# Kernel optimization log

Hardware: AMD Instinct MI355X
Metric: run time of the kernel (lower is better)

The kernel has to match this reference:

```python
import jax, jax.numpy as jnp
import numpy as np

B, T, D, P = 4, 2048, 1024, 128

def setup_inputs() -> dict:
    key = jax.random.key(0)
    ks = jax.random.split(key, 10)
    inp = {
        "x": jax.random.normal(ks[0], (B, T, D), dtype=jnp.float32),
        "Q_filt": jax.random.normal(ks[1], (P, P), dtype=jnp.float32),
        "K_filt": jax.random.normal(ks[2], (P, P), dtype=jnp.float32),
        "W_in": jax.random.normal(ks[3], (D, P), dtype=jnp.float32) / np.sqrt(D),
        "b_in": jax.random.normal(ks[4], (P,), dtype=jnp.float32) * 0.01,
        "W_v": jax.random.normal(ks[5], (D, P), dtype=jnp.float32) / np.sqrt(D),
        "b_v": jax.random.normal(ks[6], (P,), dtype=jnp.float32) * 0.01,
        "W_o": jax.random.normal(ks[7], (P, D), dtype=jnp.float32) / np.sqrt(P),
        "b_o": jax.random.normal(ks[8], (D,), dtype=jnp.float32) * 0.01,
        "decay": jnp.ones((T,), dtype=jnp.float32),
    }
    return inp

def reference(x, Q_filt, K_filt, W_in, b_in, W_v, b_v, W_o, b_o, decay):
    # x: (B,T,D)
    x_proj = x @ W_in + b_in          # (B,T,P)
    Q = x_proj @ Q_filt               # (B,T,P)
    K = x_proj @ K_filt               # (B,T,P)
    V = x @ W_v + b_v                 # (B,T,P)
    # outer-product state per timestep, scaled by per-step decay
    Z = jnp.einsum('bti,btj->btij', V, K) * decay[None, :, None, None]
    H = jnp.cumsum(Z, axis=1)         # (B,T,P,P) cumulative linear-attn state
    Y = jnp.einsum('bti,btij->btj', Q, H)  # (B,T,P)
    return Y @ W_o + b_o              # (B,T,D)
```

## Files before the change

kernel.cpp:

```cpp
#include <hip/hip_runtime.h>

#define BB 4
#define TT 2048
#define DD 1024
#define PP 128
#define NC 16
#define CH 128

typedef __attribute__((ext_vector_type(8))) short bf16x8;
typedef __attribute__((ext_vector_type(4))) float f32x4;

__device__ inline ushort f2bf(float f) {
  unsigned u = __builtin_bit_cast(unsigned, f);
  u = (u + 0x7FFF + ((u >> 16) & 1)) >> 16;
  return (ushort)u;
}

__device__ inline void gll16(const void* g, void* l) {
  __builtin_amdgcn_global_load_lds(
      (const __attribute__((address_space(1))) void*)g,
      (__attribute__((address_space(3))) void*)l, 16, 0, 0);
}

__device__ inline int swzoff(int row, int kbyte) {
  return row * 256 + (kbyte ^ ((row & 7) << 4));
}
__device__ inline int swz128(int row, int kbyte) {
  return row * 128 + (kbyte ^ ((row & 7) << 4));
}

template <int NI, int NT>
__device__ inline void stage_swz(const ushort* __restrict__ g, int ld, int koff,
                                 char* lds, int tid) {
#pragma unroll
  for (int j = 0; j < NI; ++j) {
    int L = j * (NT * 16) + tid * 16;
    int row = L >> 8;
    int off = (L & 255) ^ ((row & 7) << 4);
    gll16(g + (size_t)row * ld + koff + (off >> 1),
          lds + j * (NT * 16) + ((tid & (NT - 64)) << 4));
  }
}
template <int NI, int NT>
__device__ inline void stage_swz128(const ushort* __restrict__ g, int ld,
                                    int koff, char* lds, int tid) {
#pragma unroll
  for (int j = 0; j < NI; ++j) {
    int L = j * (NT * 16) + tid * 16;
    int row = L >> 7;
    int off = (L & 127) ^ ((row & 7) << 4);
    gll16(g + (size_t)row * ld + koff + (off >> 1),
          lds + j * (NT * 16) + ((tid & (NT - 64)) << 4));
  }
}

__device__ inline bf16x8 ld_swz(const char* lds, int row, int kbyte) {
  return *(const bf16x8*)(lds + swzoff(row, kbyte));
}
__device__ inline bf16x8 ld_swz128(const char* lds, int row, int kbyte) {
  return *(const bf16x8*)(lds + swz128(row, kbyte));
}

__device__ inline bf16x8 pack8(const float4& a, const float4& b) {
  bf16x8 v;
  v[0] = (short)f2bf(a.x); v[1] = (short)f2bf(a.y);
  v[2] = (short)f2bf(a.z); v[3] = (short)f2bf(a.w);
  v[4] = (short)f2bf(b.x); v[5] = (short)f2bf(b.y);
  v[6] = (short)f2bf(b.z); v[7] = (short)f2bf(b.w);
  return v;
}

__global__ __launch_bounds__(256) void prep_t(
    const float* __restrict__ Qf, const float* __restrict__ Kf,
    const float* __restrict__ W_in, const float* __restrict__ b_in,
    const float* __restrict__ W_v, const float* __restrict__ b_v,
    const float* __restrict__ W_o, ushort* __restrict__ WcatT,
    ushort* __restrict__ QKcT, ushort* __restrict__ WoT,
    float* __restrict__ bcat) {
  const int bid = blockIdx.x;
  const int t = threadIdx.x;
  if (bid == 104) {
    bcat[t] = (t < 128) ? b_in[t] : b_v[t - 128];
    return;
  }
  const float* src;
  ushort* dst;
  int ld_src, ld_dst, nn0;
  if (bid < 64) {
    int tn = bid >> 4, tk = bid & 15;
    src = (tn < 2) ? W_in : W_v;
    nn0 = (tn & 1) * 64;
    ld_src = 128;
    src += (size_t)(tk * 64) * 128;
    dst = WcatT + (size_t)(tn * 64) * 1024 + tk * 64;
    ld_dst = 1024;
  } else if (bid < 96) {
    int j = bid - 64, tn = j >> 1, tk = j & 1;
    src = W_o;
    nn0 = tn * 64;
    ld_src = 1024;
    src += (size_t)(tk * 64) * 1024;
    dst = WoT + (size_t)(tn * 64) * 128 + tk * 64;
    ld_dst = 128;
  } else {
    int j = bid - 96, tn = j >> 1, tk = j & 1;
    src = (tn < 2) ? Qf : Kf;
    nn0 = (tn & 1) * 64;
    ld_src = 128;
    src += (size_t)(tk * 64) * 128;
    dst = QKcT + (size_t)(tn * 64) * 128 + tk * 64;
    ld_dst = 128;
  }
  __shared__ ushort Tt[64][68];
  const int kr = t >> 4, nc = (t & 15) * 4;
#pragma unroll
  for (int p = 0; p < 4; ++p) {
    float4 v = *(const float4*)&src[(size_t)(p * 16 + kr) * ld_src + nn0 + nc];
    Tt[p * 16 + kr][nc + 0] = f2bf(v.x);
    Tt[p * 16 + kr][nc + 1] = f2bf(v.y);
    Tt[p * 16 + kr][nc + 2] = f2bf(v.z);
    Tt[p * 16 + kr][nc + 3] = f2bf(v.w);
  }
  __syncthreads();
  const int nr = t >> 4, kc = (t & 15) * 4;
#pragma unroll
  for (int p = 0; p < 4; ++p) {
    ushort4 o;
    o.x = Tt[kc + 0][p * 16 + nr];
    o.y = Tt[kc + 1][p * 16 + nr];
    o.z = Tt[kc + 2][p * 16 + nr];
    o.w = Tt[kc + 3][p * 16 + nr];
    *(ushort4*)&dst[(size_t)(p * 16 + nr) * ld_dst + kc] = o;
  }
}

__global__ __launch_bounds__(512) void gemm_xw(
    const float* __restrict__ x, const ushort* __restrict__ WcatT,
    const ushort* __restrict__ QKcT, const float* __restrict__ bcat,
    const float* __restrict__ decay, ushort* __restrict__ Qb,
    ushort* __restrict__ KdT, ushort* __restrict__ V,
    ushort* __restrict__ VT) {
  __shared__ char sm[81920];
  const int bid = blockIdx.x;
  const int swz = (bid & 7) * 32 + (bid >> 3);
  const int bm = (swz >> 1) * 64;
  const int bn = (swz & 1) * 128;
  const int tid = threadIdx.x, w = tid >> 6, l = tid & 63;
  const int wr = w >> 2, wc = w & 3, lr = l & 15, lk = l >> 4;

  const int arow = tid >> 3;
  const int acol = (tid & 7) * 8;
  const float* Ax = x + (size_t)(bm + arow) * DD + acol;
  const ushort* Bg = WcatT + (size_t)bn * DD;

  float4 ra[2];
  f32x4 z = {0.f, 0.f, 0.f, 0.f};
  f32x4 acc[2][2];
#pragma unroll
  for (int m = 0; m < 2; ++m)
#pragma unroll
    for (int n = 0; n < 2; ++n) acc[m][n] = z;

#define LOADA(t)                                                 \
  {                                                              \
    const float4* p = (const float4*)(Ax + (((t) & 15) << 6));   \
    ra[0] = p[0];                                                \
    ra[1] = p[1];                                                \
  }
#define WRITEA(lds) \
  { *(bf16x8*)((lds) + swz128(arow, acol * 2)) = pack8(ra[0], ra[1]); }

  LOADA(0);
  stage_swz128<2, 512>(Bg, DD, 0, sm + 8192, tid);
  asm volatile("s_waitcnt vmcnt(2)" ::: "memory");
  WRITEA(sm);
  LOADA(1);

  int cur = 0;
  for (int t = 0; t < 16; ++t) {
    char* nxt = sm + (cur ^ 1) * 24576;
    stage_swz128<2, 512>(Bg, DD, ((t + 1) & 15) << 6, nxt + 8192, tid);
    asm volatile("s_waitcnt vmcnt(2)" ::: "memory");
    WRITEA(nxt);
    LOADA(t + 2);
    asm volatile("s_waitcnt lgkmcnt(0)" ::: "memory");
    __builtin_amdgcn_s_barrier();
    const char* cp = sm + cur * 24576;
#pragma unroll
    for (int ks = 0; ks < 2; ++ks) {
      const int kb = ks * 64 + lk * 16;
      bf16x8 af[2], bfp[2];
#pragma unroll
      for (int m = 0; m < 2; ++m)
        af[m] = ld_swz128(cp, wr * 32 + m * 16 + lr, kb);
#pragma unroll
      for (int n = 0; n < 2; ++n)
        bfp[n] = ld_swz128(cp + 8192, wc * 32 + n * 16 + lr, kb);
#pragma unroll
      for (int m = 0; m < 2; ++m)
#pragma unroll
        for (int n = 0; n < 2; ++n)
          acc[m][n] = __builtin_amdgcn_mfma_f32_16x16x32_bf16(af[m], bfp[n], acc[m][n], 0, 0, 0);
    }
    __builtin_amdgcn_s_barrier();
    cur ^= 1;
  }
  asm volatile("s_waitcnt vmcnt(0)" ::: "memory");
  __syncthreads();
#undef LOADA
#undef WRITEA

  if (bn == 0) {
#pragma unroll
    for (int m = 0; m < 2; ++m)
#pragma unroll
      for (int n = 0; n < 2; ++n) {
        const int rowl = wr * 32 + m * 16 + lk * 4;
        const int col = wc * 32 + n * 16 + lr;
        const float bv = bcat[col];
#pragma unroll
        for (int j = 0; j < 4; ++j)
          *(ushort*)(sm + swzoff(rowl + j, col * 2)) = f2bf(acc[m][n][j] + bv);
      }
    stage_swz<8, 512>(QKcT, PP, 0, sm + 16384, tid);
    __syncthreads();

    f32x4 a2[2][4];
#pragma unroll
    for (int m = 0; m < 2; ++m)
#pragma unroll
      for (int n = 0; n < 4; ++n) a2[m][n] = z;
#pragma unroll
    for (int ks = 0; ks < 4; ++ks) {
      const int kb = ks * 64 + lk * 16;
      bf16x8 af[2], bfp[4];
#pragma unroll
      for (int m = 0; m < 2; ++m)
        af[m] = ld_swz(sm, wr * 32 + m * 16 + lr, kb);
#pragma unroll
      for (int n = 0; n < 4; ++n)
        bfp[n] = ld_swz(sm + 16384, wc * 64 + n * 16 + lr, kb);
#pragma unroll
      for (int m = 0; m < 2; ++m)
#pragma unroll
        for (int n = 0; n < 4; ++n)
          a2[m][n] = __builtin_amdgcn_mfma_f32_16x16x32_bf16(af[m], bfp[n], a2[m][n], 0, 0, 0);
    }
    __syncthreads();

#pragma unroll
    for (int m = 0; m < 2; ++m)
#pragma unroll
      for (int n = 0; n < 4; ++n) {
        const int rowl = wr * 32 + m * 16 + lk * 4;
        const int col = wc * 64 + n * 16 + lr;
        if (col < 128) {
#pragma unroll
          for (int j = 0; j < 4; ++j)
            Qb[(size_t)(bm + rowl + j) * PP + col] = f2bf(a2[m][n][j]);
        } else {
          const int cc = col - 128;
#pragma unroll
          for (int j = 0; j < 4; ++j) {
            float v = a2[m][n][j] * decay[(bm + rowl + j) & (TT - 1)];
            *(ushort*)(sm + swz128(cc, (rowl + j) * 2)) = f2bf(v);
          }
        }
      }
    __syncthreads();

    {
      const int cc = tid >> 2;
#pragma unroll
      for (int i = 0; i < 2; ++i) {
        const int ch = (tid & 3) * 2 + i;
        bf16x8 v = ld_swz128(sm, cc, ch * 16);
        *(bf16x8*)&KdT[(size_t)cc * (BB * TT) + bm + ch * 8] = v;
      }
    }
  } else {
    ushort(*VTt)[72] = (ushort(*)[72]) & sm[0];
#pragma unroll
    for (int m = 0; m < 2; ++m)
#pragma unroll
      for (int n = 0; n < 2; ++n) {
        const int tl = wr * 32 + m * 16 + lk * 4;
        const int cc = wc * 32 + n * 16 + lr;
        const float bv = bcat[128 + cc];
#pragma unroll
        for (int j = 0; j < 4; ++j) {
          ushort u = f2bf(acc[m][n][j] + bv);
          V[(size_t)(bm + tl + j) * PP + cc] = u;
          VTt[cc][tl + j] = u;
        }
      }
    __syncthreads();
    const int row = tid >> 2;
#pragma unroll
    for (int i = 0; i < 2; ++i) {
      const int ch = (tid & 3) * 2 + i;
      bf16x8 v = *(const bf16x8*)&VTt[row][ch * 8];
      *(bf16x8*)&VT[(size_t)row * (BB * TT) + bm + ch * 8] = v;
    }
  }
}

__global__ __launch_bounds__(256) void chunk_state(
    const ushort* __restrict__ KdT, const ushort* __restrict__ VT,
    float* __restrict__ Sc) {
  const int p = blockIdx.x;
  const int xcd = p & 7, idx = p >> 3;
  const int bc = xcd + 8 * (idx >> 2);
  const int q = idx & 3;
  const int qj = q >> 1, qi = q & 1;
  const size_t r0 = (size_t)(bc >> 4) * TT + (bc & 15) * CH;
  const int tid = threadIdx.x, w = tid >> 6, l = tid & 63;
  const int wr = w >> 1, wc = w & 1, lr = l & 15, lk = l >> 4;

  f32x4 z = {0.f, 0.f, 0.f, 0.f};
  f32x4 acc[2][2];
#pragma unroll
  for (int m = 0; m < 2; ++m)
#pragma unroll
    for (int n = 0; n < 2; ++n) acc[m][n] = z;
#pragma unroll
  for (int ks = 0; ks < 4; ++ks) {
    const int kk = ks * 32 + lk * 8;
    bf16x8 af[2], bf[2];
#pragma unroll
    for (int m = 0; m < 2; ++m)
      af[m] = *(const bf16x8*)&KdT[(size_t)(qj * 64 + wr * 32 + m * 16 + lr) * (BB * TT) + r0 + kk];
#pragma unroll
    for (int n = 0; n < 2; ++n)
      bf[n] = *(const bf16x8*)&VT[(size_t)(qi * 64 + wc * 32 + n * 16 + lr) * (BB * TT) + r0 + kk];
#pragma unroll
    for (int m = 0; m < 2; ++m)
#pragma unroll
      for (int n = 0; n < 2; ++n)
        acc[m][n] = __builtin_amdgcn_mfma_f32_16x16x32_bf16(af[m], bf[n], acc[m][n], 0, 0, 0);
  }
#pragma unroll
  for (int m = 0; m < 2; ++m)
#pragma unroll
    for (int n = 0; n < 2; ++n)
#pragma unroll
      for (int j = 0; j < 4; ++j)
        Sc[(size_t)bc * 16384 +
           (size_t)(qj * 64 + wr * 32 + m * 16 + lk * 4 + j) * 128 +
           (qi * 64 + wc * 32 + n * 16 + lr)] = acc[m][n][j];
}

__global__ __launch_bounds__(256) void chunk_scan(const float* __restrict__ Sc,
                                                  ushort* __restrict__ SxT) {
  const int b = blockIdx.y;
  const int e = blockIdx.x * 256 + threadIdx.x;
  float run = 0.f;
#pragma unroll
  for (int c = 0; c < NC; ++c) {
    const size_t idx = (size_t)(b * NC + c) * 16384 + e;
    SxT[idx] = f2bf(run);
    run += Sc[idx];
  }
}

__global__ __launch_bounds__(256) void attn_mfma(
    const ushort* __restrict__ Qb, const ushort* __restrict__ V,
    const ushort* __restrict__ KdT, const ushort* __restrict__ SxT,
    ushort* __restrict__ Y) {
  __shared__ char Am[64 * 256];
  const int p = blockIdx.x;
  const int xcd = p & 7, idx = p >> 3;
  const int bc = xcd + 8 * (idx >> 2);
  const int q = idx & 3;
  const int hr = q >> 1, hc = q & 1;
  const size_t r0 = (size_t)(bc >> 4) * TT + (bc & 15) * CH;
  const int tid = threadIdx.x, w = tid >> 6, l = tid & 63;
  const int wr = w >> 1, wc = w & 1, lr = l & 15, lk = l >> 4;

  f32x4 z = {0.f, 0.f, 0.f, 0.f};
  f32x4 a1[2][4];
#pragma unroll
  for (int m = 0; m < 2; ++m)
#pragma unroll
    for (int n = 0; n < 4; ++n) a1[m][n] = z;

#pragma unroll
  for (int ks = 0; ks < 4; ++ks) {
    const int kk = ks * 32 + lk * 8;
    bf16x8 af[2], bf[4];
#pragma unroll
    for (int m = 0; m < 2; ++m)
      af[m] = *(const bf16x8*)&Qb[(r0 + hr * 64 + wr * 32 + m * 16 + lr) * 128 + kk];
#pragma unroll
    for (int n = 0; n < 4; ++n)
      bf[n] = *(const bf16x8*)&V[(r0 + wc * 64 + n * 16 + lr) * 128 + kk];
#pragma unroll
    for (int m = 0; m < 2; ++m)
#pragma unroll
      for (int n = 0; n < 4; ++n)
        a1[m][n] = __builtin_amdgcn_mfma_f32_16x16x32_bf16(af[m], bf[n], a1[m][n], 0, 0, 0);
  }
#pragma unroll
  for (int m = 0; m < 2; ++m)
#pragma unroll
    for (int n = 0; n < 4; ++n)
#pragma unroll
      for (int j = 0; j < 4; ++j) {
        int tl = wr * 32 + m * 16 + lk * 4 + j;
        int t = hr * 64 + tl;
        int s = wc * 64 + n * 16 + lr;
        float v = (s <= t) ? a1[m][n][j] : 0.f;
        *(ushort*)(Am + swzoff(tl, s * 2)) = f2bf(v);
      }
  __syncthreads();

  f32x4 a2[2][2];
#pragma unroll
  for (int m = 0; m < 2; ++m)
#pragma unroll
    for (int n = 0; n < 2; ++n) a2[m][n] = z;
#pragma unroll
  for (int ks = 0; ks < 4; ++ks) {
    const int kb = ks * 64 + lk * 16, kk = ks * 32 + lk * 8;
    bf16x8 af[2], bf[2];
#pragma unroll
    for (int m = 0; m < 2; ++m)
      af[m] = ld_swz(Am, wr * 32 + m * 16 + lr, kb);
#pragma unroll
    for (int n = 0; n < 2; ++n)
      bf[n] = *(const bf16x8*)&KdT[(size_t)(hc * 64 + wc * 32 + n * 16 + lr) * (BB * TT) + r0 + kk];
#pragma unroll
    for (int m = 0; m < 2; ++m)
#pragma unroll
      for (int n = 0; n < 2; ++n)
        a2[m][n] = __builtin_amdgcn_mfma_f32_16x16x32_bf16(af[m], bf[n], a2[m][n], 0, 0, 0);
  }
#pragma unroll
  for (int ks = 0; ks < 4; ++ks) {
    const int kk = ks * 32 + lk * 8;
    bf16x8 af[2], bf[2];
#pragma unroll
    for (int m = 0; m < 2; ++m)
      af[m] = *(const bf16x8*)&Qb[(r0 + hr * 64 + wr * 32 + m * 16 + lr) * 128 + kk];
#pragma unroll
    for (int n = 0; n < 2; ++n)
      bf[n] = *(const bf16x8*)&SxT[(size_t)bc * 16384 +
                                   (size_t)(hc * 64 + wc * 32 + n * 16 + lr) * 128 + kk];
#pragma unroll
    for (int m = 0; m < 2; ++m)
#pragma unroll
      for (int n = 0; n < 2; ++n)
        a2[m][n] = __builtin_amdgcn_mfma_f32_16x16x32_bf16(af[m], bf[n], a2[m][n], 0, 0, 0);
  }
#pragma unroll
  for (int m = 0; m < 2; ++m)
#pragma unroll
    for (int n = 0; n < 2; ++n)
#pragma unroll
      for (int j = 0; j < 4; ++j) {
        int t = hr * 64 + wr * 32 + m * 16 + lk * 4 + j;
        int col = hc * 64 + wc * 32 + n * 16 + lr;
        Y[(r0 + t) * 128 + col] = f2bf(a2[m][n][j]);
      }
}

__global__ __launch_bounds__(256) void gemm_out(
    const ushort* __restrict__ Y, const ushort* __restrict__ WoT,
    const float* __restrict__ b_o, float* __restrict__ out) {
  __shared__ char sm[49152];
  const int bid = blockIdx.x;
  const int swz = (bid & 7) * 128 + (bid >> 3);
  const int bm = (swz >> 3) * 64, bn = (swz & 7) * 128;
  const int tid = threadIdx.x, w = tid >> 6, l = tid & 63;
  const int wr = w >> 1, wc = w & 1, lr = l & 15, lk = l >> 4;
  stage_swz<4, 256>(Y + (size_t)bm * PP, PP, 0, sm, tid);
  stage_swz<8, 256>(WoT + (size_t)bn * PP, PP, 0, sm + 16384, tid);
  f32x4 z = {0.f, 0.f, 0.f, 0.f};
  f32x4 acc[2][4];
#pragma unroll
  for (int m = 0; m < 2; ++m)
#pragma unroll
    for (int n = 0; n < 4; ++n) acc[m][n] = z;
  __syncthreads();
#pragma unroll
  for (int ks = 0; ks < 4; ++ks) {
    const int kb = ks * 64 + lk * 16;
    bf16x8 af[2], bfp[4];
#pragma unroll
    for (int m = 0; m < 2; ++m) af[m] = ld_swz(sm, wr * 32 + m * 16 + lr, kb);
#pragma unroll
    for (int n = 0; n < 4; ++n)
      bfp[n] = ld_swz(sm + 16384, wc * 64 + n * 16 + lr, kb);
#pragma unroll
    for (int m = 0; m < 2; ++m)
#pragma unroll
      for (int n = 0; n < 4; ++n)
        acc[m][n] = __builtin_amdgcn_mfma_f32_16x16x32_bf16(af[m], bfp[n], acc[m][n], 0, 0, 0);
  }
#pragma unroll
  for (int m = 0; m < 2; ++m)
#pragma unroll
    for (int n = 0; n < 4; ++n) {
      const int rowb = bm + wr * 32 + m * 16 + lk * 4;
      const int col = bn + wc * 64 + n * 16 + lr;
      const float bv = b_o[col];
#pragma unroll
      for (int j = 0; j < 4; ++j)
        out[(size_t)(rowb + j) * DD + col] = acc[m][n][j] + bv;
    }
}

extern "C" void kernel_launch(void* const* d_in, const int* in_sizes, int n_in,
                              void* d_out, int out_size, void* d_ws, size_t ws_size,
                              hipStream_t stream) {
  const float* x = (const float*)d_in[0];
  const float* Qf = (const float*)d_in[1];
  const float* Kf = (const float*)d_in[2];
  const float* W_in = (const float*)d_in[3];
  const float* b_in = (const float*)d_in[4];
  const float* W_v = (const float*)d_in[5];
  const float* b_v = (const float*)d_in[6];
  const float* W_o = (const float*)d_in[7];
  const float* b_o = (const float*)d_in[8];
  const float* decay = (const float*)d_in[9];
  float* out = (float*)d_out;
  char* W = (char*)d_ws;

  ushort* V     = (ushort*)(W);
  ushort* VT    = (ushort*)(W + 2097152);
  ushort* Qb    = (ushort*)(W + 4194304);
  ushort* KdT   = (ushort*)(W + 6291456);
  float*  Sc    = (float*)(W + 8388608);
  ushort* SxT   = (ushort*)(W + 12582912);
  ushort* Yb    = (ushort*)(W + 14680064);
  ushort* WcatT = (ushort*)(W + 16777216);
  ushort* QKcT  = (ushort*)(W + 17301504);
  ushort* WoT   = (ushort*)(W + 17367040);
  float*  bcat  = (float*)(W + 17629184);

  prep_t<<<105, 256, 0, stream>>>(Qf, Kf, W_in, b_in, W_v, b_v, W_o,
                                  WcatT, QKcT, WoT, bcat);
  gemm_xw<<<256, 512, 0, stream>>>(x, WcatT, QKcT, bcat, decay,
                                   Qb, KdT, V, VT);
  chunk_state<<<256, 256, 0, stream>>>(KdT, VT, Sc);
  chunk_scan<<<dim3(64, BB), 256, 0, stream>>>(Sc, SxT);
  attn_mfma<<<256, 256, 0, stream>>>(Qb, V, KdT, SxT, Yb);
  gemm_out<<<1024, 256, 0, stream>>>(Yb, WoT, b_o, out);
}
```

Baseline: 48.78 us.

## Fuse chunk state and scan into one kernel, shrink gemm_xw LDS

```diff
diff --git a/kernel.cpp b/kernel.cpp
--- a/kernel.cpp
+++ b/kernel.cpp
@@ -134,13 +134,13 @@
   }
 }
 
-__global__ __launch_bounds__(512) void gemm_xw(
+__global__ __launch_bounds__(512, 4) void gemm_xw(
     const float* __restrict__ x, const ushort* __restrict__ WcatT,
     const ushort* __restrict__ QKcT, const float* __restrict__ bcat,
     const float* __restrict__ decay, ushort* __restrict__ Qb,
     ushort* __restrict__ KdT, ushort* __restrict__ V,
     ushort* __restrict__ VT) {
-  __shared__ char sm[81920];
+  __shared__ char sm[49152];
   const int bid = blockIdx.x;
   const int swz = (bid & 7) * 32 + (bid >> 3);
   const int bm = (swz >> 1) * 64;
@@ -222,7 +222,6 @@
         for (int j = 0; j < 4; ++j)
           *(ushort*)(sm + swzoff(rowl + j, col * 2)) = f2bf(acc[m][n][j] + bv);
       }
-    stage_swz<8, 512>(QKcT, PP, 0, sm + 16384, tid);
     __syncthreads();
 
     f32x4 a2[2][4];
@@ -232,14 +231,14 @@
       for (int n = 0; n < 4; ++n) a2[m][n] = z;
 #pragma unroll
     for (int ks = 0; ks < 4; ++ks) {
-      const int kb = ks * 64 + lk * 16;
+      const int kb = ks * 64 + lk * 16, kk = ks * 32 + lk * 8;
       bf16x8 af[2], bfp[4];
 #pragma unroll
       for (int m = 0; m < 2; ++m)
         af[m] = ld_swz(sm, wr * 32 + m * 16 + lr, kb);
 #pragma unroll
       for (int n = 0; n < 4; ++n)
-        bfp[n] = ld_swz(sm + 16384, wc * 64 + n * 16 + lr, kb);
+        bfp[n] = *(const bf16x8*)&QKcT[(size_t)(wc * 64 + n * 16 + lr) * PP + kk];
 #pragma unroll
       for (int m = 0; m < 2; ++m)
 #pragma unroll
@@ -263,7 +262,7 @@
 #pragma unroll
           for (int j = 0; j < 4; ++j) {
             float v = a2[m][n][j] * decay[(bm + rowl + j) & (TT - 1)];
-            *(ushort*)(sm + swz128(cc, (rowl + j) * 2)) = f2bf(v);
+            *(ushort*)(sm + 16384 + swz128(cc, (rowl + j) * 2)) = f2bf(v);
           }
         }
       }
@@ -274,7 +273,7 @@
 #pragma unroll
       for (int i = 0; i < 2; ++i) {
         const int ch = (tid & 3) * 2 + i;
-        bf16x8 v = ld_swz128(sm, cc, ch * 16);
+        bf16x8 v = ld_swz128(sm + 16384, cc, ch * 16);
         *(bf16x8*)&KdT[(size_t)cc * (BB * TT) + bm + ch * 8] = v;
       }
     }
@@ -305,61 +304,31 @@
   }
 }
 
-__global__ __launch_bounds__(256) void chunk_state(
+__global__ __launch_bounds__(256) void state_scan(
     const ushort* __restrict__ KdT, const ushort* __restrict__ VT,
-    float* __restrict__ Sc) {
+    ushort* __restrict__ SxT) {
   const int p = blockIdx.x;
-  const int xcd = p & 7, idx = p >> 3;
-  const int bc = xcd + 8 * (idx >> 2);
-  const int q = idx & 3;
-  const int qj = q >> 1, qi = q & 1;
-  const size_t r0 = (size_t)(bc >> 4) * TT + (bc & 15) * CH;
+  const int b = p >> 4, qj = (p >> 2) & 3, qi = p & 3;
   const int tid = threadIdx.x, w = tid >> 6, l = tid & 63;
-  const int wr = w >> 1, wc = w & 1, lr = l & 15, lk = l >> 4;
-
-  f32x4 z = {0.f, 0.f, 0.f, 0.f};
-  f32x4 acc[2][2];
-#pragma unroll
-  for (int m = 0; m < 2; ++m)
-#pragma unroll
-    for (int n = 0; n < 2; ++n) acc[m][n] = z;
-#pragma unroll
-  for (int ks = 0; ks < 4; ++ks) {
-    const int kk = ks * 32 + lk * 8;
-    bf16x8 af[2], bf[2];
-#pragma unroll
-    for (int m = 0; m < 2; ++m)
-      af[m] = *(const bf16x8*)&KdT[(size_t)(qj * 64 + wr * 32 + m * 16 + lr) * (BB * TT) + r0 + kk];
-#pragma unroll
-    for (int n = 0; n < 2; ++n)
-      bf[n] = *(const bf16x8*)&VT[(size_t)(qi * 64 + wc * 32 + n * 16 + lr) * (BB * TT) + r0 + kk];
-#pragma unroll
-    for (int m = 0; m < 2; ++m)
-#pragma unroll
-      for (int n = 0; n < 2; ++n)
-        acc[m][n] = __builtin_amdgcn_mfma_f32_16x16x32_bf16(af[m], bf[n], acc[m][n], 0, 0, 0);
-  }
-#pragma unroll
-  for (int m = 0; m < 2; ++m)
-#pragma unroll
-    for (int n = 0; n < 2; ++n)
-#pragma unroll
-      for (int j = 0; j < 4; ++j)
-        Sc[(size_t)bc * 16384 +
-           (size_t)(qj * 64 + wr * 32 + m * 16 + lk * 4 + j) * 128 +
-           (qi * 64 + wc * 32 + n * 16 + lr)] = acc[m][n][j];
-}
-
-__global__ __launch_bounds__(256) void chunk_scan(const float* __restrict__ Sc,
-                                                  ushort* __restrict__ SxT) {
-  const int b = blockIdx.y;
-  const int e = blockIdx.x * 256 + threadIdx.x;
-  float run = 0.f;
-#pragma unroll
+  const int wj = w >> 1, wi = w & 1, lr = l & 15, lk = l >> 4;
+  const int jb = qj * 32 + wj * 16;
+  const int ib = qi * 32 + wi * 16;
+
+  f32x4 acc = {0.f, 0.f, 0.f, 0.f};
+#pragma unroll 2
   for (int c = 0; c < NC; ++c) {
-    const size_t idx = (size_t)(b * NC + c) * 16384 + e;
-    SxT[idx] = f2bf(run);
-    run += Sc[idx];
+    const size_t base = (size_t)(b * NC + c) * 16384;
+#pragma unroll
+    for (int j = 0; j < 4; ++j)
+      SxT[base + (size_t)(jb + lk * 4 + j) * 128 + ib + lr] = f2bf(acc[j]);
+    const size_t r0 = (size_t)b * TT + c * CH;
+#pragma unroll
+    for (int ks = 0; ks < 4; ++ks) {
+      const int kk = ks * 32 + lk * 8;
+      bf16x8 af = *(const bf16x8*)&KdT[(size_t)(jb + lr) * (BB * TT) + r0 + kk];
+      bf16x8 bf = *(const bf16x8*)&VT[(size_t)(ib + lr) * (BB * TT) + r0 + kk];
+      acc = __builtin_amdgcn_mfma_f32_16x16x32_bf16(af, bf, acc, 0, 0, 0);
+    }
   }
 }
 
@@ -530,20 +499,18 @@
   ushort* VT    = (ushort*)(W + 2097152);
   ushort* Qb    = (ushort*)(W + 4194304);
   ushort* KdT   = (ushort*)(W + 6291456);
-  float*  Sc    = (float*)(W + 8388608);
-  ushort* SxT   = (ushort*)(W + 12582912);
-  ushort* Yb    = (ushort*)(W + 14680064);
-  ushort* WcatT = (ushort*)(W + 16777216);
-  ushort* QKcT  = (ushort*)(W + 17301504);
-  ushort* WoT   = (ushort*)(W + 17367040);
-  float*  bcat  = (float*)(W + 17629184);
+  ushort* SxT   = (ushort*)(W + 8388608);
+  ushort* Yb    = (ushort*)(W + 10485760);
+  ushort* WcatT = (ushort*)(W + 12582912);
+  ushort* QKcT  = (ushort*)(W + 13107200);
+  ushort* WoT   = (ushort*)(W + 13172736);
+  float*  bcat  = (float*)(W + 13434880);
 
   prep_t<<<105, 256, 0, stream>>>(Qf, Kf, W_in, b_in, W_v, b_v, W_o,
                                   WcatT, QKcT, WoT, bcat);
   gemm_xw<<<256, 512, 0, stream>>>(x, WcatT, QKcT, bcat, decay,
                                    Qb, KdT, V, VT);
-  chunk_state<<<256, 256, 0, stream>>>(KdT, VT, Sc);
-  chunk_scan<<<dim3(64, BB), 256, 0, stream>>>(Sc, SxT);
+  state_scan<<<64, 256, 0, stream>>>(KdT, VT, SxT);
   attn_mfma<<<256, 256, 0, stream>>>(Qb, V, KdT, SxT, Yb);
   gemm_out<<<1024, 256, 0, stream>>>(Yb, WoT, b_o, out);
 }
```

Measured after the change: 60.59 us. 24.2% more time.

## Split Q/K filter GEMM into two passes to shrink LDS and raise occupancy

Applied to the files above, without the earlier changes.

```diff
diff --git a/kernel.cpp b/kernel.cpp
--- a/kernel.cpp
+++ b/kernel.cpp
@@ -134,13 +134,13 @@
   }
 }
 
-__global__ __launch_bounds__(512) void gemm_xw(
+__global__ __launch_bounds__(512, 4) void gemm_xw(
     const float* __restrict__ x, const ushort* __restrict__ WcatT,
     const ushort* __restrict__ QKcT, const float* __restrict__ bcat,
     const float* __restrict__ decay, ushort* __restrict__ Qb,
     ushort* __restrict__ KdT, ushort* __restrict__ V,
     ushort* __restrict__ VT) {
-  __shared__ char sm[81920];
+  __shared__ char sm[49152];
   const int bid = blockIdx.x;
   const int swz = (bid & 7) * 32 + (bid >> 3);
   const int bm = (swz >> 1) * 64;
@@ -222,49 +222,77 @@
         for (int j = 0; j < 4; ++j)
           *(ushort*)(sm + swzoff(rowl + j, col * 2)) = f2bf(acc[m][n][j] + bv);
       }
-    stage_swz<8, 512>(QKcT, PP, 0, sm + 16384, tid);
+    stage_swz<4, 512>(QKcT, PP, 0, sm + 16384, tid);
     __syncthreads();
-
-    f32x4 a2[2][4];
-#pragma unroll
-    for (int m = 0; m < 2; ++m)
-#pragma unroll
-      for (int n = 0; n < 4; ++n) a2[m][n] = z;
+    {
+      f32x4 aq[2][2];
+#pragma unroll
+      for (int m = 0; m < 2; ++m)
+#pragma unroll
+        for (int n = 0; n < 2; ++n) aq[m][n] = z;
+#pragma unroll
+      for (int ks = 0; ks < 4; ++ks) {
+        const int kb = ks * 64 + lk * 16;
+        bf16x8 af[2], bfp[2];
+#pragma unroll
+        for (int m = 0; m < 2; ++m)
+          af[m] = ld_swz(sm, wr * 32 + m * 16 + lr, kb);
+#pragma unroll
+        for (int n = 0; n < 2; ++n)
+          bfp[n] = ld_swz(sm + 16384, wc * 32 + n * 16 + lr, kb);
+#pragma unroll
+        for (int m = 0; m < 2; ++m)
+#pragma unroll
+          for (int n = 0; n < 2; ++n)
+            aq[m][n] = __builtin_amdgcn_mfma_f32_16x16x32_bf16(af[m], bfp[n], aq[m][n], 0, 0, 0);
+      }
+#pragma unroll
+      for (int m = 0; m < 2; ++m)
+#pragma unroll
+        for (int n = 0; n < 2; ++n) {
+          const int rowl = wr * 32 + m * 16 + lk * 4;
+          const int col = wc * 32 + n * 16 + lr;
+#pragma unroll
+          for (int j = 0; j < 4; ++j)
+            Qb[(size_t)(bm + rowl + j) * PP + col] = f2bf(aq[m][n][j]);
+        }
+    }
+    __syncthreads();
+    stage_swz<4, 512>(QKcT + (size_t)128 * PP, PP, 0, sm + 16384, tid);
+    __syncthreads();
+    f32x4 ak[2][2];
+#pragma unroll
+    for (int m = 0; m < 2; ++m)
+#pragma unroll
+      for (int n = 0; n < 2; ++n) ak[m][n] = z;
 #pragma unroll
     for (int ks = 0; ks < 4; ++ks) {
       const int kb = ks * 64 + lk * 16;
-      bf16x8 af[2], bfp[4];
+      bf16x8 af[2], bfp[2];
 #pragma unroll
       for (int m = 0; m < 2; ++m)
         af[m] = ld_swz(sm, wr * 32 + m * 16 + lr, kb);
 #pragma unroll
-      for (int n = 0; n < 4; ++n)
-        bfp[n] = ld_swz(sm + 16384, wc * 64 + n * 16 + lr, kb);
+      for (int n = 0; n < 2; ++n)
+        bfp[n] = ld_swz(sm + 16384, wc * 32 + n * 16 + lr, kb);
 #pragma unroll
       for (int m = 0; m < 2; ++m)
 #pragma unroll
-        for (int n = 0; n < 4; ++n)
-          a2[m][n] = __builtin_amdgcn_mfma_f32_16x16x32_bf16(af[m], bfp[n], a2[m][n], 0, 0, 0);
+        for (int n = 0; n < 2; ++n)
+          ak[m][n] = __builtin_amdgcn_mfma_f32_16x16x32_bf16(af[m], bfp[n], ak[m][n], 0, 0, 0);
     }
     __syncthreads();
 
 #pragma unroll
     for (int m = 0; m < 2; ++m)
 #pragma unroll
-      for (int n = 0; n < 4; ++n) {
+      for (int n = 0; n < 2; ++n) {
         const int rowl = wr * 32 + m * 16 + lk * 4;
-        const int col = wc * 64 + n * 16 + lr;
-        if (col < 128) {
-#pragma unroll
-          for (int j = 0; j < 4; ++j)
-            Qb[(size_t)(bm + rowl + j) * PP + col] = f2bf(a2[m][n][j]);
-        } else {
-          const int cc = col - 128;
-#pragma unroll
-          for (int j = 0; j < 4; ++j) {
-            float v = a2[m][n][j] * decay[(bm + rowl + j) & (TT - 1)];
-            *(ushort*)(sm + swz128(cc, (rowl + j) * 2)) = f2bf(v);
-          }
+        const int cc = wc * 32 + n * 16 + lr;
+#pragma unroll
+        for (int j = 0; j < 4; ++j) {
+          float v = ak[m][n][j] * decay[(bm + rowl + j) & (TT - 1)];
+          *(ushort*)(sm + 16384 + swz128(cc, (rowl + j) * 2)) = f2bf(v);
         }
       }
     __syncthreads();
@@ -274,7 +302,7 @@
 #pragma unroll
       for (int i = 0; i < 2; ++i) {
         const int ch = (tid & 3) * 2 + i;
-        bf16x8 v = ld_swz128(sm, cc, ch * 16);
+        bf16x8 v = ld_swz128(sm + 16384, cc, ch * 16);
         *(bf16x8*)&KdT[(size_t)cc * (BB * TT) + bm + ch * 8] = v;
       }
     }
```

Result: slower. 50.25 us (+3.0%).

## Retile x-projection GEMM to full-width 32-row tiles computing x_proj and V together

Applied to the files above, without the earlier changes.

```diff
diff --git a/kernel.cpp b/kernel.cpp
--- a/kernel.cpp
+++ b/kernel.cpp
@@ -28,6 +28,9 @@
 __device__ inline int swz128(int row, int kbyte) {
   return row * 128 + (kbyte ^ ((row & 7) << 4));
 }
+__device__ inline int swz64(int row, int kbyte) {
+  return row * 64 + (kbyte ^ ((row & 3) << 4));
+}
 
 template <int NI, int NT>
 __device__ inline void stage_swz(const ushort* __restrict__ g, int ld, int koff,
@@ -59,15 +62,6 @@
 }
 __device__ inline bf16x8 ld_swz128(const char* lds, int row, int kbyte) {
   return *(const bf16x8*)(lds + swz128(row, kbyte));
-}
-
-__device__ inline bf16x8 pack8(const float4& a, const float4& b) {
-  bf16x8 v;
-  v[0] = (short)f2bf(a.x); v[1] = (short)f2bf(a.y);
-  v[2] = (short)f2bf(a.z); v[3] = (short)f2bf(a.w);
-  v[4] = (short)f2bf(b.x); v[5] = (short)f2bf(b.y);
-  v[6] = (short)f2bf(b.z); v[7] = (short)f2bf(b.w);
-  return v;
 }
 
 __global__ __launch_bounds__(256) void prep_t(
@@ -140,20 +134,16 @@
     const float* __restrict__ decay, ushort* __restrict__ Qb,
     ushort* __restrict__ KdT, ushort* __restrict__ V,
     ushort* __restrict__ VT) {
-  __shared__ char sm[81920];
-  const int bid = blockIdx.x;
-  const int swz = (bid & 7) * 32 + (bid >> 3);
-  const int bm = (swz >> 1) * 64;
-  const int bn = (swz & 1) * 128;
+  __shared__ char sm[84992];
+  const int bm = blockIdx.x * 32;
   const int tid = threadIdx.x, w = tid >> 6, l = tid & 63;
-  const int wr = w >> 2, wc = w & 3, lr = l & 15, lk = l >> 4;
-
-  const int arow = tid >> 3;
-  const int acol = (tid & 7) * 8;
+  const int lr = l & 15, lk = l >> 4;
+
+  const int arow = tid >> 4;
+  const int acol = (tid & 15) * 4;
   const float* Ax = x + (size_t)(bm + arow) * DD + acol;
-  const ushort* Bg = WcatT + (size_t)bn * DD;
-
-  float4 ra[2];
+
+  float4 ra;
   f32x4 z = {0.f, 0.f, 0.f, 0.f};
   f32x4 acc[2][2];
 #pragma unroll
@@ -161,41 +151,41 @@
 #pragma unroll
     for (int n = 0; n < 2; ++n) acc[m][n] = z;
 
-#define LOADA(t)                                                 \
+#define LOADA(t) { ra = *(const float4*)(Ax + (((t) & 15) << 6)); }
+#define WRITEA(lds)                                              \
   {                                                              \
-    const float4* p = (const float4*)(Ax + (((t) & 15) << 6));   \
-    ra[0] = p[0];                                                \
-    ra[1] = p[1];                                                \
-  }
-#define WRITEA(lds) \
-  { *(bf16x8*)((lds) + swz128(arow, acol * 2)) = pack8(ra[0], ra[1]); }
+    ushort4 pk;                                                  \
+    pk.x = f2bf(ra.x); pk.y = f2bf(ra.y);                        \
+    pk.z = f2bf(ra.z); pk.w = f2bf(ra.w);                        \
+    *(ushort4*)((lds) + swz128(arow, acol * 2)) = pk;            \
+  }
 
   LOADA(0);
-  stage_swz128<2, 512>(Bg, DD, 0, sm + 8192, tid);
-  asm volatile("s_waitcnt vmcnt(2)" ::: "memory");
+  stage_swz128<4, 512>(WcatT, DD, 0, sm + 4096, tid);
+  asm volatile("s_waitcnt vmcnt(4)" ::: "memory");
   WRITEA(sm);
   LOADA(1);
 
   int cur = 0;
   for (int t = 0; t < 16; ++t) {
-    char* nxt = sm + (cur ^ 1) * 24576;
-    stage_swz128<2, 512>(Bg, DD, ((t + 1) & 15) << 6, nxt + 8192, tid);
-    asm volatile("s_waitcnt vmcnt(2)" ::: "memory");
+    char* nxt = sm + (cur ^ 1) * 36864;
+    stage_swz128<4, 512>(WcatT, DD, ((t + 1) & 15) << 6, nxt + 4096, tid);
+    asm volatile("s_waitcnt vmcnt(4)" ::: "memory");
     WRITEA(nxt);
     LOADA(t + 2);
     asm volatile("s_waitcnt lgkmcnt(0)" ::: "memory");
     __builtin_amdgcn_s_barrier();
-    const char* cp = sm + cur * 24576;
+    const char* cp = sm + cur * 36864;
 #pragma unroll
     for (int ks = 0; ks < 2; ++ks) {
       const int kb = ks * 64 + lk * 16;
       bf16x8 af[2], bfp[2];
 #pragma unroll
       for (int m = 0; m < 2; ++m)
-        af[m] = ld_swz128(cp, wr * 32 + m * 16 + lr, kb);
+        af[m] = ld_swz128(cp, m * 16 + lr, kb);
 #pragma unroll
       for (int n = 0; n < 2; ++n)
-        bfp[n] = ld_swz128(cp + 8192, wc * 32 + n * 16 + lr, kb);
+        bfp[n] = ld_swz128(cp + 4096, w * 32 + n * 16 + lr, kb);
 #pragma unroll
       for (int m = 0; m < 2; ++m)
 #pragma unroll
@@ -210,98 +200,85 @@
 #undef LOADA
 #undef WRITEA
 
-  if (bn == 0) {
-#pragma unroll
-    for (int m = 0; m < 2; ++m)
-#pragma unroll
-      for (int n = 0; n < 2; ++n) {
-        const int rowl = wr * 32 + m * 16 + lk * 4;
-        const int col = wc * 32 + n * 16 + lr;
-        const float bv = bcat[col];
+  ushort(*VTt)[40] = (ushort(*)[40]) & sm[73728];
+#pragma unroll
+  for (int m = 0; m < 2; ++m)
+#pragma unroll
+    for (int n = 0; n < 2; ++n) {
+      const int rowl = m * 16 + lk * 4;
+      const int col = w * 32 + n * 16 + lr;
+      const float bv = bcat[col];
+      if (col < 128) {
 #pragma unroll
         for (int j = 0; j < 4; ++j)
           *(ushort*)(sm + swzoff(rowl + j, col * 2)) = f2bf(acc[m][n][j] + bv);
-      }
-    stage_swz<8, 512>(QKcT, PP, 0, sm + 16384, tid);
-    __syncthreads();
-
-    f32x4 a2[2][4];
-#pragma unroll
-    for (int m = 0; m < 2; ++m)
-#pragma unroll
-      for (int n = 0; n < 4; ++n) a2[m][n] = z;
-#pragma unroll
-    for (int ks = 0; ks < 4; ++ks) {
-      const int kb = ks * 64 + lk * 16;
-      bf16x8 af[2], bfp[4];
-#pragma unroll
-      for (int m = 0; m < 2; ++m)
-        af[m] = ld_swz(sm, wr * 32 + m * 16 + lr, kb);
-#pragma unroll
-      for (int n = 0; n < 4; ++n)
-        bfp[n] = ld_swz(sm + 16384, wc * 64 + n * 16 + lr, kb);
-#pragma unroll
-      for (int m = 0; m < 2; ++m)
-#pragma unroll
-        for (int n = 0; n < 4; ++n)
-          a2[m][n] = __builtin_amdgcn_mfma_f32_16x16x32_bf16(af[m], bfp[n], a2[m][n], 0, 0, 0);
-    }
-    __syncthreads();
-
-#pragma unroll
-    for (int m = 0; m < 2; ++m)
-#pragma unroll
-      for (int n = 0; n < 4; ++n) {
-        const int rowl = wr * 32 + m * 16 + lk * 4;
-        const int col = wc * 64 + n * 16 + lr;
-        if (col < 128) {
-#pragma unroll
-          for (int j = 0; j < 4; ++j)
-            Qb[(size_t)(bm + rowl + j) * PP + col] = f2bf(a2[m][n][j]);
-        } else {
-          const int cc = col - 128;
-#pragma unroll
-          for (int j = 0; j < 4; ++j) {
-            float v = a2[m][n][j] * decay[(bm + rowl + j) & (TT - 1)];
-            *(ushort*)(sm + swz128(cc, (rowl + j) * 2)) = f2bf(v);
-          }
+      } else {
+        const int cc = col - 128;
+#pragma unroll
+        for (int j = 0; j < 4; ++j) {
+          ushort u = f2bf(acc[m][n][j] + bv);
+          V[(size_t)(bm + rowl + j) * PP + cc] = u;
+          VTt[cc][rowl + j] = u;
         }
       }
-    __syncthreads();
-
-    {
-      const int cc = tid >> 2;
-#pragma unroll
-      for (int i = 0; i < 2; ++i) {
-        const int ch = (tid & 3) * 2 + i;
-        bf16x8 v = ld_swz128(sm, cc, ch * 16);
-        *(bf16x8*)&KdT[(size_t)cc * (BB * TT) + bm + ch * 8] = v;
+    }
+  stage_swz<8, 512>(QKcT, PP, 0, sm + 8192, tid);
+  __syncthreads();
+
+  {
+    const int cc = tid >> 2, ch = tid & 3;
+    bf16x8 v = *(const bf16x8*)&VTt[cc][ch * 8];
+    *(bf16x8*)&VT[(size_t)cc * (BB * TT) + bm + ch * 8] = v;
+  }
+
+  f32x4 aq[2][2];
+#pragma unroll
+  for (int m = 0; m < 2; ++m)
+#pragma unroll
+    for (int n = 0; n < 2; ++n) aq[m][n] = z;
+#pragma unroll
+  for (int ks = 0; ks < 4; ++ks) {
+    const int kb = ks * 64 + lk * 16;
+    bf16x8 af[2], bfp[2];
+#pragma unroll
+    for (int m = 0; m < 2; ++m)
+      af[m] = ld_swz(sm, m * 16 + lr, kb);
+#pragma unroll
+    for (int n = 0; n < 2; ++n)
+      bfp[n] = ld_swz(sm + 8192, w * 32 + n * 16 + lr, kb);
+#pragma unroll
+    for (int m = 0; m < 2; ++m)
+#pragma unroll
+      for (int n = 0; n < 2; ++n)
+        aq[m][n] = __builtin_amdgcn_mfma_f32_16x16x32_bf16(af[m], bfp[n], aq[m][n], 0, 0, 0);
+  }
+  __syncthreads();
+
+#pragma unroll
+  for (int m = 0; m < 2; ++m)
+#pragma unroll
+    for (int n = 0; n < 2; ++n) {
+      const int rowl = m * 16 + lk * 4;
+      const int col = w * 32 + n * 16 + lr;
+      if (col < 128) {
+#pragma unroll
+        for (int j = 0; j < 4; ++j)
+          Qb[(size_t)(bm + rowl + j) * PP + col] = f2bf(aq[m][n][j]);
+      } else {
+        const int cc = col - 128;
+#pragma unroll
+        for (int j = 0; j < 4; ++j) {
+          float v = aq[m][n][j] * decay[(bm + rowl + j) & (TT - 1)];
+          *(ushort*)(sm + swz64(cc, (rowl + j) * 2)) = f2bf(v);
+        }
       }
     }
-  } else {
-    ushort(*VTt)[72] = (ushort(*)[72]) & sm[0];
-#pragma unroll
-    for (int m = 0; m < 2; ++m)
-#pragma unroll
-      for (int n = 0; n < 2; ++n) {
-        const int tl = wr * 32 + m * 16 + lk * 4;
-        const int cc = wc * 32 + n * 16 + lr;
-        const float bv = bcat[128 + cc];
-#pragma unroll
-        for (int j = 0; j < 4; ++j) {
-          ushort u = f2bf(acc[m][n][j] + bv);
-          V[(size_t)(bm + tl + j) * PP + cc] = u;
-          VTt[cc][tl + j] = u;
-        }
-      }
-    __syncthreads();
-    const int row = tid >> 2;
-#pragma unroll
-    for (int i = 0; i < 2; ++i) {
-      const int ch = (tid & 3) * 2 + i;
-      bf16x8 v = *(const bf16x8*)&VTt[row][ch * 8];
-      *(bf16x8*)&VT[(size_t)row * (BB * TT) + bm + ch * 8] = v;
-    }
+  __syncthreads();
+
+  {
+    const int cc = tid >> 2, ch = tid & 3;
+    bf16x8 v = *(const bf16x8*)(sm + swz64(cc, ch * 16));
+    *(bf16x8*)&KdT[(size_t)cc * (BB * TT) + bm + ch * 8] = v;
   }
 }
 
```

After: 54.68 us. +12.1%, slower.
